# Kernel optimization log

Measured on AMD Instinct MI355X. Metric: run time of the kernel, lower is better.

## Reference

```python
import jax, jax.numpy as jnp
import numpy as np

B, S, D, H = 2, 2048, 1024, 16
EPS = 1e-7  # keras backend epsilon

def setup_inputs() -> dict:
    key = jax.random.key(0)
    ks = jax.random.split(key, 5)
    x = jax.random.normal(ks[0], (B, S, D), dtype=jnp.float32)
    # mem_mask convention: attend where mem_mask == 0 (causal here)
    i = jnp.arange(S)
    causal = (i[None, :] > i[:, None]).astype(jnp.float32)  # 1 = masked
    mem_mask = jnp.broadcast_to(causal[None, None], (B, 1, S, S))
    Wqkv = jax.random.normal(ks[1], (D, 3 * D), dtype=jnp.float32) * (D ** -0.5)
    W_out = jax.random.normal(ks[2], (D, D), dtype=jnp.float32) * (D ** -0.5)
    b_out = jnp.zeros((D,), dtype=jnp.float32)
    scale = jnp.ones((D,), dtype=jnp.float32)
    gate = jax.random.normal(ks[3], (D,), dtype=jnp.float32) * 0.02
    return {"x": x, "mem_mask": mem_mask, "Wqkv": Wqkv, "W_out": W_out,
            "b_out": b_out, "scale": scale, "gate": gate}

def reference(x, mem_mask, Wqkv, W_out, b_out, scale, gate):
    b, s, d = x.shape
    dh = d // H
    h = jnp.einsum('bsd,de->bse', x, Wqkv)
    q, k, v = jnp.split(h, 3, axis=-1)
    def split_heads(t):
        return t.reshape(b, s, H, dh).transpose(0, 2, 1, 3)  # [B,H,S,dh]
    q, k, v = split_heads(q), split_heads(k), split_heads(v)
    q = q * (dh ** -0.5)
    logits = jnp.einsum('bhqd,bhkd->bhqk', q, k)
    logits = logits * (mem_mask == 0.0).astype(logits.dtype)
    weights = jax.nn.relu(logits)
    o = jnp.einsum('bhqk,bhkd->bhqd', weights, v)
    o = o.transpose(0, 2, 1, 3).reshape(b, s, d)  # combine heads
    # Gated RMSNorm
    ms = jnp.mean(o * o, axis=-1, keepdims=True)
    o = scale * o * jax.lax.rsqrt(ms + EPS) * jax.nn.sigmoid(gate * o)
    return jnp.einsum('bsd,de->bse', o, W_out) + b_out
```

## Files before the change

kernel.cpp:

```cpp
#include <hip/hip_runtime.h>
#include <hip/hip_bf16.h>

typedef unsigned short u16;
typedef __attribute__((ext_vector_type(8))) short bf16x8;
typedef __attribute__((ext_vector_type(4))) short short4v;
typedef __attribute__((ext_vector_type(4))) float floatx4;
typedef __attribute__((ext_vector_type(2))) unsigned uint2v;
typedef __attribute__((ext_vector_type(4))) unsigned uint4v;

__device__ __forceinline__ float bf2f(u16 u) {
    unsigned v = ((unsigned)u) << 16;
    return __builtin_bit_cast(float, v);
}
__device__ __forceinline__ u16 f2bf(float f) {
    unsigned u = __builtin_bit_cast(unsigned, f);
    u += 0x7fffu + ((u >> 16) & 1u);
    return (u16)(u >> 16);
}

#define GLDS16(g, l)                                                             \
    __builtin_amdgcn_global_load_lds(                                            \
        (const __attribute__((address_space(1))) void*)(g),                      \
        (__attribute__((address_space(3))) void*)(l), 16, 0, 0)

__device__ __forceinline__ uint2v pl32(unsigned a, unsigned b) {
#if __has_builtin(__builtin_amdgcn_permlane32_swap)
    auto r = __builtin_amdgcn_permlane32_swap(a, b, false, false);
    uint2v o; o.x = (unsigned)r[0]; o.y = (unsigned)r[1]; return o;
#else
    unsigned as = (unsigned)__shfl_xor((int)a, 32, 64);
    unsigned bs = (unsigned)__shfl_xor((int)b, 32, 64);
    const bool hi = (threadIdx.x & 32) != 0;
    uint2v o; o.x = hi ? bs : a; o.y = hi ? b : as; return o;
#endif
}
__device__ __forceinline__ uint2v pl16(unsigned a, unsigned b) {
#if __has_builtin(__builtin_amdgcn_permlane16_swap)
    auto r = __builtin_amdgcn_permlane16_swap(a, b, false, false);
    uint2v o; o.x = (unsigned)r[0]; o.y = (unsigned)r[1]; return o;
#else
    unsigned as = (unsigned)__shfl_xor((int)a, 16, 64);
    unsigned bs = (unsigned)__shfl_xor((int)b, 16, 64);
    const bool odd = (threadIdx.x & 16) != 0;
    uint2v o; o.x = odd ? bs : a; o.y = odd ? b : as; return o;
#endif
}

__global__ __launch_bounds__(256) void prep(const float* __restrict__ x, u16* __restrict__ xb,
                                            const float* __restrict__ Wqkv, u16* __restrict__ WqkvT,
                                            const float* __restrict__ Wout, u16* __restrict__ WoutT) {
    __shared__ u16 t[32][33];
    int blk = blockIdx.x;
    if (blk < 4096) {
        const int i = blk * 256 + threadIdx.x;
        const floatx4 v = ((const floatx4*)x)[i];
        short4v o;
#pragma unroll
        for (int j = 0; j < 4; ++j) o[j] = (short)f2bf(v[j]);
        ((short4v*)xb)[i] = o;
        return;
    }
    const float* in; u16* out; int R, C, bx, by;
    if (blk < 4096 + 3072) { blk -= 4096; in = Wqkv; out = WqkvT; R = 1024; C = 3072; bx = blk % 96; by = blk / 96; }
    else                   { blk -= 7168; in = Wout; out = WoutT; R = 1024; C = 1024; bx = blk & 31; by = blk >> 5; }
    const int c0 = bx * 32, r0 = by * 32;
    const int xx = threadIdx.x & 31, yy = threadIdx.x >> 5;
#pragma unroll
    for (int i = 0; i < 32; i += 8) t[yy + i][xx] = f2bf(in[(size_t)(r0 + yy + i) * C + c0 + xx]);
    __syncthreads();
#pragma unroll
    for (int i = 0; i < 32; i += 8) out[(size_t)(c0 + yy + i) * R + r0 + xx] = t[xx][yy + i];
}

template <int TM, int BN, bool BIAS, typename OUT, bool VT>
__global__ __launch_bounds__(256) void gemm_bt(const u16* __restrict__ A, const u16* __restrict__ Bt,
                                               OUT* __restrict__ C, const float* __restrict__ bias,
                                               u16* __restrict__ vtp, int M, int N, int K) {
    constexpr int MI = TM / 32;
    constexpr int NJ = BN / 32;
    __shared__ u16 sA[TM * 32];
    __shared__ u16 sB[BN * 32];
    const int tid = threadIdx.x;
    const int lane = tid & 63, wave = tid >> 6;
    const int l15 = lane & 15, quad = lane >> 4;
    const int row0 = blockIdx.y * TM, col0 = blockIdx.x * BN;
    const int wm = (wave & 1) * (TM / 2), wn = (wave >> 1) * (BN / 2);
    const int c_ = (tid & 3) << 3;
    floatx4 acc[MI][NJ] = {};
    for (int k0 = 0; k0 < K; k0 += 32) {
#pragma unroll
        for (int it = 0; it < BN / 64; ++it) {
            const int idx = it * 256 + tid;
            const int r = idx >> 2;
            GLDS16(Bt + (size_t)(col0 + r) * K + k0 + c_, sB + idx * 8);
        }
#pragma unroll
        for (int it = 0; it < TM / 64; ++it) {
            const int idx = it * 256 + tid;
            const int r = idx >> 2;
            GLDS16(A + (size_t)(row0 + r) * K + k0 + c_, sA + idx * 8);
        }
        __syncthreads();
        bf16x8 af[MI], bfr[NJ];
#pragma unroll
        for (int i = 0; i < MI; ++i) af[i] = *(const bf16x8*)(sA + (wm + i * 16 + l15) * 32 + quad * 8);
#pragma unroll
        for (int j = 0; j < NJ; ++j) bfr[j] = *(const bf16x8*)(sB + (wn + j * 16 + l15) * 32 + quad * 8);
#pragma unroll
        for (int i = 0; i < MI; ++i)
#pragma unroll
            for (int j = 0; j < NJ; ++j)
                acc[i][j] = __builtin_amdgcn_mfma_f32_16x16x32_bf16(af[i], bfr[j], acc[i][j], 0, 0, 0);
        __syncthreads();
    }
#pragma unroll
    for (int i = 0; i < MI; ++i) {
#pragma unroll
        for (int j = 0; j < NJ; ++j) {
            const int col = col0 + wn + j * 16 + l15;
            const int row = row0 + wm + i * 16 + quad * 4;
            const float b = BIAS ? bias[col] : 0.f;
            short4v pk;
#pragma unroll
            for (int r = 0; r < 4; ++r) {
                const float v = acc[i][j][r] + b;
                if constexpr (sizeof(OUT) == 2)
                    C[(size_t)(row + r) * N + col] = (OUT)f2bf(v);
                else
                    C[(size_t)(row + r) * N + col] = (OUT)v;
                if constexpr (VT) pk[r] = (short)f2bf(v * 0.125f);
            }
            if constexpr (VT) {
                if (col0 >= 2048) {
                    const int bb = row >> 11, s = row & 2047;
                    const int hd = (col - 2048) >> 6, dh = col & 63;
                    *(short4v*)(vtp + ((size_t)(bb * 16 + hd) * 64 + dh) * 2048 + s) = pk;
                }
            }
        }
    }
}

__device__ __forceinline__ uint2v pack_relu(floatx4 s, bool diag, int kgb, int qg) {
    float v0 = fmaxf(s[0], 0.f), v1 = fmaxf(s[1], 0.f);
    float v2 = fmaxf(s[2], 0.f), v3 = fmaxf(s[3], 0.f);
    if (diag) {
        if (kgb + 0 > qg) v0 = 0.f;
        if (kgb + 1 > qg) v1 = 0.f;
        if (kgb + 2 > qg) v2 = 0.f;
        if (kgb + 3 > qg) v3 = 0.f;
    }
    uint2v p;
    p.x = ((__builtin_bit_cast(unsigned, v0) + 0x8000u) >> 16) |
          ((__builtin_bit_cast(unsigned, v1) + 0x8000u) & 0xffff0000u);
    p.y = ((__builtin_bit_cast(unsigned, v2) + 0x8000u) >> 16) |
          ((__builtin_bit_cast(unsigned, v3) + 0x8000u) & 0xffff0000u);
    return p;
}

__device__ __forceinline__ bf16x8 pfrag(uint2v A, uint2v B) {
    uint2v gx = pl32(A.x, B.x);
    uint2v dx = pl16(gx.x, gx.y);
    uint2v gy = pl32(A.y, B.y);
    uint2v dy = pl16(gy.x, gy.y);
    uint4v w; w.x = dx.x; w.y = dy.x; w.z = dx.y; w.w = dy.y;
    return __builtin_bit_cast(bf16x8, w);
}

__global__ __launch_bounds__(256, 2) void relu_attn(const u16* __restrict__ h, const u16* __restrict__ vt,
                                                    float* __restrict__ o) {
    union SM {
        struct { u16 K[2][128 * 64]; u16 V[2][64 * 128]; } kv;
        float red[4][64 * 68];
    };
    __shared__ SM sm;
    const int bid = blockIdx.x;
    const int pr = bid >> 5;
    const int bh = bid & 31;
    const int qt64 = 31 - pr;
    const int b = bh >> 4, hd = bh & 15;
    const int tid = threadIdx.x, lane = tid & 63, wave = tid >> 6;
    const int l15 = lane & 15, quad = lane >> 4;
    const int nc = (qt64 >> 1) + 1;

    const int qrow0 = b * 2048 + qt64 * 64;
    bf16x8 qf[4][2];
#pragma unroll
    for (int qt = 0; qt < 4; ++qt)
#pragma unroll
        for (int ks = 0; ks < 2; ++ks)
            qf[qt][ks] = *(const bf16x8*)(h + (size_t)(qrow0 + qt * 16 + l15) * 3072 + hd * 64 + ks * 32 + quad * 8);

    floatx4 acc[4][4] = {};

    const u16* kbase = h + (size_t)(b * 2048) * 3072 + 1024 + hd * 64;
    const u16* vbase = vt + (size_t)bh * 64 * 2048;

    const u16* kq[4]; const u16* vq[4]; int klo[4], vlo[4];
#pragma unroll
    for (int it = 0; it < 4; ++it) {
        const int idx = it * 256 + tid;
        { const int r = idx >> 3, c = idx & 7, cg = c ^ (r & 7);
          kq[it] = kbase + (size_t)r * 3072 + cg * 8; klo[it] = idx * 8; }
        { const int r = idx >> 4, c = idx & 15, cg = c ^ (r & 15);
          vq[it] = vbase + (size_t)r * 2048 + cg * 8; vlo[it] = idx * 8; }
    }
    auto stage = [&](int bufi) {
#pragma unroll
        for (int it = 0; it < 4; ++it) { GLDS16(kq[it], &sm.kv.K[bufi][klo[it]]); kq[it] += 128 * 3072; }
#pragma unroll
        for (int it = 0; it < 4; ++it) { GLDS16(vq[it], &sm.kv.V[bufi][vlo[it]]); vq[it] += 128; }
    };

    stage(0);
    int buf = 0;
    for (int kc = 0; kc < nc; ++kc) {
        asm volatile("s_waitcnt vmcnt(0)" ::: "memory");
        __builtin_amdgcn_s_barrier();
        asm volatile("" ::: "memory");
        __builtin_amdgcn_sched_barrier(0);
        if (kc + 1 < nc) stage(buf ^ 1);

        const u16* sK = sm.kv.K[buf];
        const u16* sV = sm.kv.V[buf];
        __builtin_amdgcn_s_setprio(1);
        bf16x8 kf[2][2];
#pragma unroll
        for (int kt = 0; kt < 2; ++kt)
#pragma unroll
            for (int ks = 0; ks < 2; ++ks) {
                const int row = wave * 32 + kt * 16 + l15;
                const int blk = (quad + ks * 4) ^ (row & 7);
                kf[kt][ks] = *(const bf16x8*)(sK + row * 64 + blk * 8);
            }
        const floatx4 z = {0.f, 0.f, 0.f, 0.f};
        floatx4 s[2][4];
#pragma unroll
        for (int kt = 0; kt < 2; ++kt)
#pragma unroll
            for (int qt = 0; qt < 4; ++qt) {
                floatx4 t = __builtin_amdgcn_mfma_f32_16x16x32_bf16(kf[kt][0], qf[qt][0], z, 0, 0, 0);
                s[kt][qt] = __builtin_amdgcn_mfma_f32_16x16x32_bf16(kf[kt][1], qf[qt][1], t, 0, 0, 0);
            }
        const bool last = (kc == nc - 1);
        uint2v p[2][4];
#pragma unroll
        for (int kt = 0; kt < 2; ++kt)
#pragma unroll
            for (int qt = 0; qt < 4; ++qt)
                p[kt][qt] = pack_relu(s[kt][qt], last,
                                      kc * 128 + wave * 32 + kt * 16 + quad * 4,
                                      qt64 * 64 + qt * 16 + l15);
        bf16x8 vf[4];
#pragma unroll
        for (int nt = 0; nt < 4; ++nt) {
            const int row = nt * 16 + l15;
            const int blk = (wave * 4 + quad) ^ (row & 15);
            vf[nt] = *(const bf16x8*)(sV + row * 128 + blk * 8);
        }
#pragma unroll
        for (int qt = 0; qt < 4; ++qt) {
            const bf16x8 pa = pfrag(p[0][qt], p[1][qt]);
#pragma unroll
            for (int nt = 0; nt < 4; ++nt)
                acc[qt][nt] = __builtin_amdgcn_mfma_f32_16x16x32_bf16(pa, vf[nt], acc[qt][nt], 0, 0, 0);
        }
        __builtin_amdgcn_s_setprio(0);
        buf ^= 1;
    }

    __syncthreads();
    float* rw = sm.red[wave];
#pragma unroll
    for (int qt = 0; qt < 4; ++qt)
#pragma unroll
        for (int nt = 0; nt < 4; ++nt) {
            const int d = nt * 16 + l15, q = qt * 16 + quad * 4;
            *(floatx4*)(rw + d * 68 + q) = acc[qt][nt];
        }
    __syncthreads();
    {
        const int d = lane;
#pragma unroll
        for (int j = 0; j < 4; ++j) {
            const int q = wave * 16 + j * 4;
            floatx4 a = *(const floatx4*)(sm.red[0] + d * 68 + q);
            a += *(const floatx4*)(sm.red[1] + d * 68 + q);
            a += *(const floatx4*)(sm.red[2] + d * 68 + q);
            a += *(const floatx4*)(sm.red[3] + d * 68 + q);
#pragma unroll
            for (int jj = 0; jj < 4; ++jj)
                o[(size_t)(qrow0 + q + jj) * 1024 + hd * 64 + d] = a[jj];
        }
    }
}

__global__ __launch_bounds__(256) void rms_gate(const float* __restrict__ o, const float* __restrict__ scale,
                                                const float* __restrict__ gate, u16* __restrict__ out) {
    const int row = blockIdx.x;
    const int tid = threadIdx.x;
    const floatx4* op = (const floatx4*)(o + (size_t)row * 1024);
    floatx4 v = op[tid];
    float ss = v[0] * v[0] + v[1] * v[1] + v[2] * v[2] + v[3] * v[3];
#pragma unroll
    for (int m = 32; m >= 1; m >>= 1) ss += __shfl_xor(ss, m, 64);
    __shared__ float red[4];
    if ((tid & 63) == 0) red[tid >> 6] = ss;
    __syncthreads();
    const float ms = (red[0] + red[1] + red[2] + red[3]) * (1.0f / 1024.0f);
    const float inv = rsqrtf(ms + 1e-7f);
    const int c = tid * 4;
#pragma unroll
    for (int j = 0; j < 4; ++j) {
        const float s = scale[c + j];
        const float g = gate[c + j];
        const float x = v[j];
        const float sig = 1.0f / (1.0f + __expf(-g * x));
        out[(size_t)row * 1024 + c + j] = f2bf(s * x * inv * sig);
    }
}

extern "C" void kernel_launch(void* const* d_in, const int* in_sizes, int n_in,
                              void* d_out, int out_size, void* d_ws, size_t ws_size,
                              hipStream_t stream) {
    const float* x     = (const float*)d_in[0];
    const float* Wqkv  = (const float*)d_in[2];
    const float* Wout  = (const float*)d_in[3];
    const float* bout  = (const float*)d_in[4];
    const float* scale = (const float*)d_in[5];
    const float* gate  = (const float*)d_in[6];
    float* out = (float*)d_out;

    char* p = (char*)d_ws;
    u16* xb    = (u16*)p; p += (size_t)4096 * 1024 * 2;
    u16* h     = (u16*)p; p += (size_t)4096 * 3072 * 2;
    u16* vt    = (u16*)p; p += (size_t)32 * 64 * 2048 * 2;
    u16* WqkvT = (u16*)p; p += (size_t)3072 * 1024 * 2;
    u16* WoutT = (u16*)p; p += (size_t)1024 * 1024 * 2;
    float* oat = (float*)p; p += (size_t)4096 * 1024 * 4;
    u16* onorm = (u16*)p; p += (size_t)4096 * 1024 * 2;

    prep<<<8192, 256, 0, stream>>>(x, xb, Wqkv, WqkvT, Wout, WoutT);
    gemm_bt<128, 128, false, u16, true><<<dim3(24, 32), 256, 0, stream>>>(xb, WqkvT, h, nullptr, vt, 4096, 3072, 1024);
    relu_attn<<<1024, 256, 0, stream>>>(h, vt, oat);
    rms_gate<<<4096, 256, 0, stream>>>(oat, scale, gate, onorm);
    gemm_bt<128, 64, true, float, false><<<dim3(16, 32), 256, 0, stream>>>(onorm, WoutT, out, bout, nullptr, 4096, 1024, 1024);
}
```

Measured before the change: 203.1 us.

## Add dedicated triple-buffered 256x256 QKV GEMM with swizzled LDS

Replaces the generic 128x128 QKV projection GEMM with a specialised 512-thread kernel using 256x256 tiles and a three-stage LDS ring filled by direct global-to-LDS loads. Explicit vmcnt waits overlap the next stage's loads with MFMA work, an XOR swizzle on the LDS layout aims to avoid bank conflicts, and setprio raises priority around the MFMA section. The larger tiles improve operand reuse but launch only 192 blocks and use 96KB of LDS per block, which may limit occupancy on the device.

Measured after the change: 215.1 us. +5.9%, slower.

```diff
diff --git a/kernel.cpp b/kernel.cpp
--- a/kernel.cpp
+++ b/kernel.cpp
@@ -72,10 +72,94 @@
     for (int i = 0; i < 32; i += 8) out[(size_t)(c0 + yy + i) * R + r0 + xx] = t[xx][yy + i];
 }
 
-template <int TM, int BN, bool BIAS, typename OUT, bool VT>
+__global__ __launch_bounds__(512, 2) void gemm_qkv(const u16* __restrict__ A, const u16* __restrict__ Bt,
+                                                   u16* __restrict__ C, u16* __restrict__ vtp) {
+    constexpr int K = 1024, N = 3072;
+    __shared__ u16 sA[3][256 * 32];
+    __shared__ u16 sB[3][256 * 32];
+    const int tid = threadIdx.x;
+    const int lane = tid & 63, wave = tid >> 6;
+    const int l15 = lane & 15, quad = lane >> 4;
+    const int row0 = blockIdx.y * 256, col0 = blockIdx.x * 256;
+    const int wm = (wave & 1) * 128, wn = (wave >> 1) * 64;
+
+    const u16* aq[2]; const u16* bq[2]; int lo[2];
+#pragma unroll
+    for (int it = 0; it < 2; ++it) {
+        const int idx = it * 512 + tid;
+        const int r = idx >> 2, bb = idx & 3;
+        const int c = bb ^ ((r >> 1) & 3);
+        aq[it] = A + (size_t)(row0 + r) * K + c * 8;
+        bq[it] = Bt + (size_t)(col0 + r) * K + c * 8;
+        lo[it] = idx * 8;
+    }
+    auto stage = [&](int bufi) {
+#pragma unroll
+        for (int it = 0; it < 2; ++it) {
+            GLDS16(aq[it], &sA[bufi][lo[it]]);
+            GLDS16(bq[it], &sB[bufi][lo[it]]);
+            aq[it] += 32; bq[it] += 32;
+        }
+    };
+
+    floatx4 acc[8][4] = {};
+    stage(0); stage(1);
+    int bc = 0, bn = 1, bs = 2;
+    for (int kc = 0; kc < 32; ++kc) {
+        if (kc < 31) asm volatile("s_waitcnt vmcnt(4)" ::: "memory");
+        else         asm volatile("s_waitcnt vmcnt(0)" ::: "memory");
+        __builtin_amdgcn_s_barrier();
+        asm volatile("" ::: "memory");
+        __builtin_amdgcn_sched_barrier(0);
+        if (kc + 2 < 32) stage(bs);
+
+        const u16* sa = sA[bc];
+        const u16* sb = sB[bc];
+        __builtin_amdgcn_s_setprio(1);
+        bf16x8 bfr[4];
+#pragma unroll
+        for (int j = 0; j < 4; ++j) {
+            const int r = wn + j * 16 + l15;
+            const int s = r * 4 + (quad ^ ((r >> 1) & 3));
+            bfr[j] = *(const bf16x8*)(sb + s * 8);
+        }
+#pragma unroll
+        for (int i = 0; i < 8; ++i) {
+            const int r = wm + i * 16 + l15;
+            const int s = r * 4 + (quad ^ ((r >> 1) & 3));
+            const bf16x8 af = *(const bf16x8*)(sa + s * 8);
+#pragma unroll
+            for (int j = 0; j < 4; ++j)
+                acc[i][j] = __builtin_amdgcn_mfma_f32_16x16x32_bf16(af, bfr[j], acc[i][j], 0, 0, 0);
+        }
+        __builtin_amdgcn_s_setprio(0);
+        int t_ = bc; bc = bn; bn = bs; bs = t_;
+    }
+#pragma unroll
+    for (int i = 0; i < 8; ++i) {
+#pragma unroll
+        for (int j = 0; j < 4; ++j) {
+            const int col = col0 + wn + j * 16 + l15;
+            const int row = row0 + wm + i * 16 + quad * 4;
+#pragma unroll
+            for (int r = 0; r < 4; ++r)
+                C[(size_t)(row + r) * N + col] = f2bf(acc[i][j][r]);
+            if (col0 >= 2048) {
+                short4v pk;
+#pragma unroll
+                for (int r = 0; r < 4; ++r) pk[r] = (short)f2bf(acc[i][j][r] * 0.125f);
+                const int bb2 = row >> 11, s = row & 2047;
+                const int hd = (col - 2048) >> 6, dh = col & 63;
+                *(short4v*)(vtp + ((size_t)(bb2 * 16 + hd) * 64 + dh) * 2048 + s) = pk;
+            }
+        }
+    }
+}
+
+template <int TM, int BN, bool BIAS, typename OUT>
 __global__ __launch_bounds__(256) void gemm_bt(const u16* __restrict__ A, const u16* __restrict__ Bt,
                                                OUT* __restrict__ C, const float* __restrict__ bias,
-                                               u16* __restrict__ vtp, int M, int N, int K) {
+                                               int M, int N, int K) {
     constexpr int MI = TM / 32;
     constexpr int NJ = BN / 32;
     __shared__ u16 sA[TM * 32];
@@ -120,7 +204,6 @@
             const int col = col0 + wn + j * 16 + l15;
             const int row = row0 + wm + i * 16 + quad * 4;
             const float b = BIAS ? bias[col] : 0.f;
-            short4v pk;
 #pragma unroll
             for (int r = 0; r < 4; ++r) {
                 const float v = acc[i][j][r] + b;
@@ -128,14 +211,6 @@
                     C[(size_t)(row + r) * N + col] = (OUT)f2bf(v);
                 else
                     C[(size_t)(row + r) * N + col] = (OUT)v;
-                if constexpr (VT) pk[r] = (short)f2bf(v * 0.125f);
-            }
-            if constexpr (VT) {
-                if (col0 >= 2048) {
-                    const int bb = row >> 11, s = row & 2047;
-                    const int hd = (col - 2048) >> 6, dh = col & 63;
-                    *(short4v*)(vtp + ((size_t)(bb * 16 + hd) * 64 + dh) * 2048 + s) = pk;
-                }
             }
         }
     }
@@ -341,8 +416,8 @@
     u16* onorm = (u16*)p; p += (size_t)4096 * 1024 * 2;
 
     prep<<<8192, 256, 0, stream>>>(x, xb, Wqkv, WqkvT, Wout, WoutT);
-    gemm_bt<128, 128, false, u16, true><<<dim3(24, 32), 256, 0, stream>>>(xb, WqkvT, h, nullptr, vt, 4096, 3072, 1024);
+    gemm_qkv<<<dim3(12, 16), 512, 0, stream>>>(xb, WqkvT, h, vt);
     relu_attn<<<1024, 256, 0, stream>>>(h, vt, oat);
     rms_gate<<<4096, 256, 0, stream>>>(oat, scale, gate, onorm);
-    gemm_bt<128, 64, true, float, false><<<dim3(16, 32), 256, 0, stream>>>(onorm, WoutT, out, bout, nullptr, 4096, 1024, 1024);
-}
+    gemm_bt<128, 64, true, float><<<dim3(16, 32), 256, 0, stream>>>(onorm, WoutT, out, bout, 4096, 1024, 1024);
+}
```
